# Optimization experiments

Measured on AMD Instinct MI355X. Metric: run time of the kernel, lower is better.

Reference implementation:

```python
import jax, jax.numpy as jnp
import numpy as np

EPS_AREA = 1e-6   # guard against zero box area in the OKS-style feedback
EPS_BCE = 1e-7    # clamp probabilities for binary cross entropy


def setup_inputs() -> dict:
    key = jax.random.key(0)
    k0, k1, k2, k3, k4 = jax.random.split(key, 5)
    L, Lp, K = 512, 64, 17
    pred_poses = jax.random.uniform(k0, (L, K, 3), dtype=jnp.float32)
    target_poses = jax.random.uniform(k1, (Lp, K, 3), dtype=jnp.float32)
    pred_feedbacks = jax.random.uniform(k2, (L,), dtype=jnp.float32)
    ious = jax.random.uniform(k3, (L, Lp), dtype=jnp.float32)
    target_areas = jax.random.uniform(k4, (Lp,), dtype=jnp.float32)
    return {
        "pred_poses": pred_poses,
        "target_poses": target_poses,
        "pred_feedbacks": pred_feedbacks,
        "ious": ious,
        "target_areas": target_areas,
        "features_dim": 56,
    }


def reference(pred_poses, target_poses, pred_feedbacks, ious, target_areas, features_dim):
    L, K, _ = pred_poses.shape
    Lp = target_poses.shape[0]

    # ---- preprocess_poses: [L, K, 3] -> [L, 3K, D, D] ----
    # Original loops over keypoints emitting torch.full maps in (x, y, v) order per
    # keypoint, which is exactly a reshape to [L, 3K] followed by spatial broadcast.
    features_poses = jnp.broadcast_to(
        pred_poses.reshape(L, 3 * K, 1, 1),
        (L, 3 * K, features_dim, features_dim),
    )

    # ---- compute_loss (interpolate_poses=False branch), fully vectorized ----
    pred_xy = pred_poses[:, :, :2]     # [L, K, 2]
    targ_xy = target_poses[:, :, :2]   # [Lp, K, 2]
    # pairwise squared keypoint distances: [L, Lp, K]
    d2 = jnp.sum((pred_xy[:, None] - targ_xy[None]) ** 2, axis=-1)
    # OKS-style target feedback per (pred, target) pair: [L, Lp]
    targ_feedback = jnp.mean(
        jnp.exp(-d2 / (2.0 * target_areas[None, :, None] + EPS_AREA)), axis=-1
    )
    # MSE feedback loss per pair
    feedback_loss = (pred_feedbacks[:, None] - targ_feedback) ** 2  # [L, Lp]

    # binary cross entropy on visibility channel, mean over K per pair
    pv = jnp.clip(pred_poses[:, :, 2], EPS_BCE, 1.0 - EPS_BCE)  # [L, K]
    tv = target_poses[:, :, 2]                                   # [Lp, K]
    bce = -(tv[None] * jnp.log(pv[:, None]) + (1.0 - tv[None]) * jnp.log(1.0 - pv[:, None]))
    bce = jnp.mean(bce, axis=-1)  # [L, Lp]

    loss = jnp.sum(ious * (feedback_loss + bce))
    return features_poses, loss
```

## Files before the change

### kernel.cpp

```cpp
#include <hip/hip_runtime.h>
#include <math.h>

#define EPS_AREA 1e-6f
#define EPS_BCE  1e-7f

typedef float v4f __attribute__((ext_vector_type(4)));

template <int INNER4>
__global__ __launch_bounds__(256) void broadcast_flat_kernel(
    const float* __restrict__ pred, float* __restrict__ out,
    unsigned int total4,
    const float* __restrict__ partial, float* __restrict__ loss_out, int L)
{
    if (blockIdx.x == 0 && threadIdx.x < 64) {
        float s = 0.0f;
        for (int i = threadIdx.x; i < L; i += 64) s += partial[i];
        for (int off = 32; off > 0; off >>= 1) s += __shfl_down(s, off, 64);
        if (threadIdx.x == 0) *loss_out = s;
    }

    v4f* dst = (v4f*)out;
    const unsigned int stride = gridDim.x * blockDim.x;
    for (unsigned int i = blockIdx.x * blockDim.x + threadIdx.x; i < total4;
         i += stride) {
        const unsigned int row = i / (unsigned int)INNER4;
        const float v = pred[row];
        v4f val;
        val.x = v; val.y = v; val.z = v; val.w = v;
        dst[i] = val;
    }
}

__global__ __launch_bounds__(256) void broadcast_rows_kernel(
    const float* __restrict__ pred, float* __restrict__ out,
    int rows, long inner, int inner4)
{
    const int wave = threadIdx.x >> 6;
    const int lane = threadIdx.x & 63;
    const int row  = blockIdx.x * 4 + wave;
    if (row >= rows) return;
    const float v = pred[row];
    v4f val;
    val.x = v; val.y = v; val.z = v; val.w = v;
    float* rowp = out + (size_t)row * (size_t)inner;
    v4f* dst = (v4f*)rowp;
    for (int i = lane; i < inner4; i += 64) dst[i] = val;
    const int rem = (int)(inner - (long)inner4 * 4);
    if (rem && lane < rem) rowp[(size_t)inner4 * 4 + lane] = v;
}

__global__ __launch_bounds__(256) void loss_partial4_kernel(
    const float* __restrict__ pred_poses,
    const float* __restrict__ target_poses,
    const float* __restrict__ pred_feedbacks,
    const float* __restrict__ ious,
    const float* __restrict__ target_areas,
    float* __restrict__ partial,
    int Lp, int K)
{
    extern __shared__ float sm[];
    float* px  = sm;
    float* py  = sm + K;
    float* lpv = sm + 2 * K;
    float* l1m = sm + 3 * K;
    float* red = sm + 4 * K;

    const int l    = blockIdx.x;
    const int tid  = threadIdx.x;
    const int w    = tid >> 6;
    const int lane = tid & 63;

    if (tid < K) {
        const float* p = pred_poses + ((size_t)l * K + tid) * 3;
        px[tid] = p[0];
        py[tid] = p[1];
        float pv = fminf(fmaxf(p[2], EPS_BCE), 1.0f - EPS_BCE);
        lpv[tid] = logf(pv);
        l1m[tid] = logf(1.0f - pv);
    }
    __syncthreads();

    float eS = 0.0f, bS = 0.0f;
    if (lane < Lp) {
        const float  invDen = 1.0f / (2.0f * target_areas[lane] + EPS_AREA);
        const float* t = target_poses + (size_t)lane * K * 3;
        for (int k = w; k < K; k += 4) {
            float tx = t[3 * k + 0];
            float ty = t[3 * k + 1];
            float tv = t[3 * k + 2];
            float dx = px[k] - tx;
            float dy = py[k] - ty;
            float d2 = dx * dx + dy * dy;
            eS += __expf(-d2 * invDen);
            bS += fmaf(tv, lpv[k] - l1m[k], l1m[k]);
        }
    }
    red[tid]       = eS;
    red[256 + tid] = bS;
    __syncthreads();

    if (w == 0) {
        float eSum = red[lane] + red[64 + lane] + red[128 + lane] + red[192 + lane];
        float bSum = red[256 + lane] + red[320 + lane] + red[384 + lane] + red[448 + lane];
        float val = 0.0f;
        if (lane < Lp) {
            float tf = eSum / (float)K;
            float d  = pred_feedbacks[l] - tf;
            val = ious[(size_t)l * Lp + lane] * (d * d - bSum / (float)K);
        }
        for (int off = 32; off > 0; off >>= 1) val += __shfl_down(val, off, 64);
        if (lane == 0) partial[l] = val;
    }
}

__global__ __launch_bounds__(64) void loss_partial1_kernel(
    const float* __restrict__ pred_poses, const float* __restrict__ target_poses,
    const float* __restrict__ pred_feedbacks, const float* __restrict__ ious,
    const float* __restrict__ target_areas, float* __restrict__ partial,
    int Lp, int K)
{
    extern __shared__ float sm[];
    float* px  = sm;
    float* py  = sm + K;
    float* lpv = sm + 2 * K;
    float* l1m = sm + 3 * K;

    const int l   = blockIdx.x;
    const int tid = threadIdx.x;
    if (tid < K) {
        const float* p = pred_poses + ((size_t)l * K + tid) * 3;
        px[tid] = p[0];
        py[tid] = p[1];
        float pv = fminf(fmaxf(p[2], EPS_BCE), 1.0f - EPS_BCE);
        lpv[tid] = logf(pv);
        l1m[tid] = logf(1.0f - pv);
    }
    __syncthreads();

    float acc = 0.0f;
    for (int lp = tid; lp < Lp; lp += 64) {
        const float  invDen = 1.0f / (2.0f * target_areas[lp] + EPS_AREA);
        const float* t = target_poses + (size_t)lp * K * 3;
        float eS = 0.0f, bS = 0.0f;
        for (int k = 0; k < K; ++k) {
            float dx = px[k] - t[3 * k + 0];
            float dy = py[k] - t[3 * k + 1];
            float tv = t[3 * k + 2];
            eS += __expf(-(dx * dx + dy * dy) * invDen);
            bS += fmaf(tv, lpv[k] - l1m[k], l1m[k]);
        }
        float d = pred_feedbacks[l] - eS / (float)K;
        acc += ious[(size_t)l * Lp + lp] * (d * d - bS / (float)K);
    }
    for (int off = 32; off > 0; off >>= 1) acc += __shfl_down(acc, off, 64);
    if (tid == 0) partial[l] = acc;
}

__global__ __launch_bounds__(256) void loss_reduce_kernel(
    const float* __restrict__ partial, float* __restrict__ loss_out, int L)
{
    __shared__ float wsum[4];
    float s = 0.0f;
    for (int i = threadIdx.x; i < L; i += 256) s += partial[i];
    for (int off = 32; off > 0; off >>= 1) s += __shfl_down(s, off, 64);
    if ((threadIdx.x & 63) == 0) wsum[threadIdx.x >> 6] = s;
    __syncthreads();
    if (threadIdx.x == 0) *loss_out = wsum[0] + wsum[1] + wsum[2] + wsum[3];
}

extern "C" void kernel_launch(void* const* d_in, const int* in_sizes, int n_in,
                              void* d_out, int out_size, void* d_ws, size_t ws_size,
                              hipStream_t stream) {
    const float* pred_poses     = (const float*)d_in[0];
    const float* target_poses   = (const float*)d_in[1];
    const float* pred_feedbacks = (const float*)d_in[2];
    const float* ious           = (const float*)d_in[3];
    const float* target_areas   = (const float*)d_in[4];
    float* out = (float*)d_out;

    const int L  = in_sizes[2];
    const int Lp = in_sizes[4];
    const int K  = in_sizes[0] / (3 * L);

    const long rows   = (long)L * 3 * K;
    const long inner  = ((long)out_size - 1) / rows;
    const int  inner4 = (int)(inner / 4);
    const int  rem    = (int)(inner - (long)inner4 * 4);

    float* loss_slot = out + ((size_t)out_size - 1);
    float* partial   = (float*)d_ws;

    if (Lp <= 64) {
        const size_t smem = (4 * (size_t)K + 512) * sizeof(float);
        loss_partial4_kernel<<<L, 256, smem, stream>>>(
            pred_poses, target_poses, pred_feedbacks, ious, target_areas,
            partial, Lp, K);
    } else {
        const size_t smem = 4 * (size_t)K * sizeof(float);
        loss_partial1_kernel<<<L, 64, smem, stream>>>(
            pred_poses, target_poses, pred_feedbacks, ious, target_areas,
            partial, Lp, K);
    }

    if (inner4 == 784 && rem == 0) {
        const unsigned int total4 = (unsigned int)(rows * 784);
        broadcast_flat_kernel<784><<<4096, 256, 0, stream>>>(
            pred_poses, out, total4, partial, loss_slot, L);
    } else {
        broadcast_rows_kernel<<<(int)((rows + 3) / 4), 256, 0, stream>>>(
            pred_poses, out, (int)rows, inner, inner4);
        loss_reduce_kernel<<<1, 256, 0, stream>>>(partial, loss_slot, L);
    }
}
```

Measured before the change: 335.9 us.

## Fuse pairwise loss into broadcast kernel via dedicated block zero

Removes the separate per-row loss kernel and computes the full loss inside block 0 of the broadcast kernel. Block 0 tiles predictions in shared memory and keeps the target keypoints in registers. The remaining blocks do the broadcast store, so the loss overlaps the memory-bound output write and one launch plus the workspace round trip is eliminated. The risk is that a single block serializes all loss work and could become the tail if it runs longer than the broadcast.

After: 502.1 us. +49.5%, slower.

```diff
diff --git a/kernel.cpp b/kernel.cpp
--- a/kernel.cpp
+++ b/kernel.cpp
@@ -6,28 +6,91 @@
 
 typedef float v4f __attribute__((ext_vector_type(4)));
 
-template <int INNER4>
-__global__ __launch_bounds__(256) void broadcast_flat_kernel(
-    const float* __restrict__ pred, float* __restrict__ out,
-    unsigned int total4,
-    const float* __restrict__ partial, float* __restrict__ loss_out, int L)
-{
-    if (blockIdx.x == 0 && threadIdx.x < 64) {
-        float s = 0.0f;
-        for (int i = threadIdx.x; i < L; i += 64) s += partial[i];
-        for (int off = 32; off > 0; off >>= 1) s += __shfl_down(s, off, 64);
-        if (threadIdx.x == 0) *loss_out = s;
-    }
-
-    v4f* dst = (v4f*)out;
-    const unsigned int stride = gridDim.x * blockDim.x;
-    for (unsigned int i = blockIdx.x * blockDim.x + threadIdx.x; i < total4;
-         i += stride) {
-        const unsigned int row = i / (unsigned int)INNER4;
-        const float v = pred[row];
-        v4f val;
-        val.x = v; val.y = v; val.z = v; val.w = v;
-        dst[i] = val;
+template <int L, int Lp, int K, int INNER4>
+__global__ __launch_bounds__(256) void fused_kernel(
+    const float* __restrict__ pred_poses,
+    const float* __restrict__ target_poses,
+    const float* __restrict__ pred_feedbacks,
+    const float* __restrict__ ious,
+    const float* __restrict__ target_areas,
+    float* __restrict__ out,
+    float* __restrict__ loss_slot,
+    unsigned int total4)
+{
+    const int tid = threadIdx.x;
+
+    if (blockIdx.x == 0) {
+        __shared__ float4 tile[32][K];
+        __shared__ float  wsum[4];
+        const int w    = tid >> 6;
+        const int lane = tid & 63;
+
+        float tx[K], ty[K], tv[K];
+        float invDen = 0.0f;
+        if (lane < Lp) {
+            invDen = 1.0f / (2.0f * target_areas[lane] + EPS_AREA);
+            const float* t = target_poses + (size_t)lane * K * 3;
+            #pragma unroll
+            for (int k = 0; k < K; ++k) {
+                tx[k] = t[3 * k + 0];
+                ty[k] = t[3 * k + 1];
+                tv[k] = t[3 * k + 2];
+            }
+        }
+
+        float wacc = 0.0f;
+        for (int tb = 0; tb < L / 32; ++tb) {
+            __syncthreads();
+            for (int e = tid; e < 32 * K; e += 256) {
+                const int lo = e / K;
+                const int k  = e - lo * K;
+                const float* p = pred_poses + ((size_t)(tb * 32 + lo) * K + k) * 3;
+                float4 c;
+                c.x = p[0];
+                c.y = p[1];
+                float pv = fminf(fmaxf(p[2], EPS_BCE), 1.0f - EPS_BCE);
+                c.z = logf(pv);
+                c.w = logf(1.0f - pv);
+                tile[lo][k] = c;
+            }
+            __syncthreads();
+
+            for (int lo = w; lo < 32; lo += 4) {
+                const int l = tb * 32 + lo;
+                float eS = 0.0f, bS = 0.0f;
+                #pragma unroll
+                for (int k = 0; k < K; ++k) {
+                    float4 c = tile[lo][k];
+                    float dx = c.x - tx[k];
+                    float dy = c.y - ty[k];
+                    eS += __expf(-(dx * dx + dy * dy) * invDen);
+                    bS += fmaf(tv[k], c.z - c.w, c.w);
+                }
+                float val = 0.0f;
+                if (lane < Lp) {
+                    float d = pred_feedbacks[l] - eS / (float)K;
+                    val = ious[(size_t)l * Lp + lane] * (d * d - bS / (float)K);
+                }
+                #pragma unroll
+                for (int off = 1; off < 64; off <<= 1)
+                    val += __shfl_xor(val, off, 64);
+                wacc += val;
+            }
+        }
+        if (lane == 0) wsum[w] = wacc;
+        __syncthreads();
+        if (tid == 0) *loss_slot = wsum[0] + wsum[1] + wsum[2] + wsum[3];
+    } else {
+        v4f* dst = (v4f*)out;
+        const unsigned int stride = (gridDim.x - 1) * 256u;
+        for (unsigned int i = (blockIdx.x - 1) * 256u + tid; i < total4;
+             i += stride) {
+            const unsigned int row = i / (unsigned int)INNER4;
+            const float v = pred_poses[row];
+            v4f val;
+            val.x = v; val.y = v; val.z = v; val.w = v;
+            dst[i] = val;
+        }
     }
 }
 
@@ -49,70 +112,6 @@
     if (rem && lane < rem) rowp[(size_t)inner4 * 4 + lane] = v;
 }
 
-__global__ __launch_bounds__(256) void loss_partial4_kernel(
-    const float* __restrict__ pred_poses,
-    const float* __restrict__ target_poses,
-    const float* __restrict__ pred_feedbacks,
-    const float* __restrict__ ious,
-    const float* __restrict__ target_areas,
-    float* __restrict__ partial,
-    int Lp, int K)
-{
-    extern __shared__ float sm[];
-    float* px  = sm;
-    float* py  = sm + K;
-    float* lpv = sm + 2 * K;
-    float* l1m = sm + 3 * K;
-    float* red = sm + 4 * K;
-
-    const int l    = blockIdx.x;
-    const int tid  = threadIdx.x;
-    const int w    = tid >> 6;
-    const int lane = tid & 63;
-
-    if (tid < K) {
-        const float* p = pred_poses + ((size_t)l * K + tid) * 3;
-        px[tid] = p[0];
-        py[tid] = p[1];
-        float pv = fminf(fmaxf(p[2], EPS_BCE), 1.0f - EPS_BCE);
-        lpv[tid] = logf(pv);
-        l1m[tid] = logf(1.0f - pv);
-    }
-    __syncthreads();
-
-    float eS = 0.0f, bS = 0.0f;
-    if (lane < Lp) {
-        const float  invDen = 1.0f / (2.0f * target_areas[lane] + EPS_AREA);
-        const float* t = target_poses + (size_t)lane * K * 3;
-        for (int k = w; k < K; k += 4) {
-            float tx = t[3 * k + 0];
-            float ty = t[3 * k + 1];
-            float tv = t[3 * k + 2];
-            float dx = px[k] - tx;
-            float dy = py[k] - ty;
-            float d2 = dx * dx + dy * dy;
-            eS += __expf(-d2 * invDen);
-            bS += fmaf(tv, lpv[k] - l1m[k], l1m[k]);
-        }
-    }
-    red[tid]       = eS;
-    red[256 + tid] = bS;
-    __syncthreads();
-
-    if (w == 0) {
-        float eSum = red[lane] + red[64 + lane] + red[128 + lane] + red[192 + lane];
-        float bSum = red[256 + lane] + red[320 + lane] + red[384 + lane] + red[448 + lane];
-        float val = 0.0f;
-        if (lane < Lp) {
-            float tf = eSum / (float)K;
-            float d  = pred_feedbacks[l] - tf;
-            val = ious[(size_t)l * Lp + lane] * (d * d - bSum / (float)K);
-        }
-        for (int off = 32; off > 0; off >>= 1) val += __shfl_down(val, off, 64);
-        if (lane == 0) partial[l] = val;
-    }
-}
-
 __global__ __launch_bounds__(64) void loss_partial1_kernel(
     const float* __restrict__ pred_poses, const float* __restrict__ target_poses,
     const float* __restrict__ pred_feedbacks, const float* __restrict__ ious,
@@ -145,9 +144,9 @@
         for (int k = 0; k < K; ++k) {
             float dx = px[k] - t[3 * k + 0];
             float dy = py[k] - t[3 * k + 1];
-            float tv = t[3 * k + 2];
+            float tvv = t[3 * k + 2];
             eS += __expf(-(dx * dx + dy * dy) * invDen);
-            bS += fmaf(tv, lpv[k] - l1m[k], l1m[k]);
+            bS += fmaf(tvv, lpv[k] - l1m[k], l1m[k]);
         }
         float d = pred_feedbacks[l] - eS / (float)K;
         acc += ious[(size_t)l * Lp + lp] * (d * d - bS / (float)K);
@@ -188,25 +187,18 @@
     const int  rem    = (int)(inner - (long)inner4 * 4);
 
     float* loss_slot = out + ((size_t)out_size - 1);
-    float* partial   = (float*)d_ws;
-
-    if (Lp <= 64) {
-        const size_t smem = (4 * (size_t)K + 512) * sizeof(float);
-        loss_partial4_kernel<<<L, 256, smem, stream>>>(
+
+    if (L == 512 && Lp == 64 && K == 17 && inner4 == 784 && rem == 0) {
+        const unsigned int total4 = (unsigned int)(rows * 784);
+        fused_kernel<512, 64, 17, 784><<<4097, 256, 0, stream>>>(
             pred_poses, target_poses, pred_feedbacks, ious, target_areas,
-            partial, Lp, K);
+            out, loss_slot, total4);
     } else {
+        float* partial = (float*)d_ws;
         const size_t smem = 4 * (size_t)K * sizeof(float);
         loss_partial1_kernel<<<L, 64, smem, stream>>>(
             pred_poses, target_poses, pred_feedbacks, ious, target_areas,
             partial, Lp, K);
-    }
-
-    if (inner4 == 784 && rem == 0) {
-        const unsigned int total4 = (unsigned int)(rows * 784);
-        broadcast_flat_kernel<784><<<4096, 256, 0, stream>>>(
-            pred_poses, out, total4, partial, loss_slot, L);
-    } else {
         broadcast_rows_kernel<<<(int)((rows + 3) / 4), 256, 0, stream>>>(
             pred_poses, out, (int)rows, inner, inner4);
         loss_reduce_kernel<<<1, 256, 0, stream>>>(partial, loss_slot, L);
```
